# Performance work log

Hardware: AMD Instinct MI355X
Metric: run time of the kernel (lower is better)

Reference implementation:

```python
import jax, jax.numpy as jnp
import numpy as np

B, C, K, HH, WW, D = 2, 4, 32, 96, 96, 64


def setup_inputs() -> dict:
    key = jax.random.key(0)
    k1, k2, k3, k4, k5 = jax.random.split(key, 5)
    heatmaps = jax.random.uniform(k1, (B, C, K, HH, WW), dtype=jnp.float32)
    # Projection matrices: random linear part, translation column centered at
    # (H/2, W/2, 1) so that most cube points project inside the heatmap with z>0.
    P = 5.0 * jax.random.normal(k2, (B, C, 3, 4), dtype=jnp.float32)
    center = jnp.array([HH / 2.0, WW / 2.0, 1.0], dtype=jnp.float32)
    P = P.at[:, :, :, 3].set(center + 0.1 * jax.random.normal(k3, (B, C, 3)))
    coord_cubes = jax.random.uniform(k4, (B, D, D, D, 3), dtype=jnp.float32,
                                     minval=-1.0, maxval=1.0)
    vol_confidences = jax.random.uniform(k5, (B, C, K), dtype=jnp.float32) + 0.1
    return {
        "heatmaps": heatmaps,
        "projection_matrices": P,
        "coord_cubes": coord_cubes,
        "vol_confidences": vol_confidences,
    }


def _unproject(heatmaps, P, coord_cubes, conf):
    """Vectorized port of `unprojection` with agg_type='conf'.

    heatmaps: (B,C,K,H,W); P: (B,C,3,4); coord_cubes: (B,D,D,D,3); conf: (B,C,K)
    Returns volumes (B,K,D,D,D).
    """
    b, c, k, H, W = heatmaps.shape
    d = coord_cubes.shape[1]
    n = d * d * d
    coords = coord_cubes.reshape(b, n, 3)
    homo = jnp.concatenate([coords, jnp.ones((b, n, 1), coords.dtype)], axis=-1)
    # Projective transform per camera: (B,C,N,3)
    proj = jnp.einsum('bnj,bcij->bcni', homo, P)
    z = proj[..., 2]
    invalid = z <= 0.0
    z_safe = jnp.where(z == 0.0, 1.0, z)
    u = proj[..., 0] / z_safe
    v = proj[..., 1] / z_safe
    # Normalization exactly as in the source (x divided by H, y by W)
    gx = 2.0 * (u / H - 0.5)
    gy = 2.0 * (v / W - 0.5)
    # grid_sample align_corners=True: x indexes width, y indexes height
    ix = (gx + 1.0) * 0.5 * (W - 1)
    iy = (gy + 1.0) * 0.5 * (H - 1)
    x0 = jnp.floor(ix)
    y0 = jnp.floor(iy)
    x1 = x0 + 1.0
    y1 = y0 + 1.0
    wx1 = ix - x0
    wx0 = 1.0 - wx1
    wy1 = iy - y0
    wy0 = 1.0 - wy1
    hm = heatmaps.reshape(b, c, k, H * W)

    def corner(xc, yc, w):
        inb = (xc >= 0) & (xc <= W - 1) & (yc >= 0) & (yc <= H - 1)
        xi = jnp.clip(xc, 0, W - 1).astype(jnp.int32)
        yi = jnp.clip(yc, 0, H - 1).astype(jnp.int32)
        idx = (yi * W + xi)[:, :, None, :]                  # (B,C,1,N)
        idx = jnp.broadcast_to(idx, (b, c, k, idx.shape[-1]))
        g = jnp.take_along_axis(hm, idx, axis=3)            # (B,C,K,N)
        return g * (w * inb)[:, :, None, :]

    val = (corner(x0, y0, wx0 * wy0) + corner(x1, y0, wx1 * wy0)
           + corner(x0, y1, wx0 * wy1) + corner(x1, y1, wx1 * wy1))
    val = jnp.where(invalid[:, :, None, :], 0.0, val)       # zero invalid voxels
    # 'conf' aggregation; confidences normalized over cameras as in forward()
    conf_n = conf / conf.sum(axis=1, keepdims=True)
    vol = (val * conf_n[..., None]).sum(axis=1)             # (B,K,N)
    return vol.reshape(b, k, d, d, d)


def reference(heatmaps, projection_matrices, coord_cubes, vol_confidences):
    return _unproject(heatmaps, projection_matrices, coord_cubes, vol_confidences)
```

## Files before the change

### kernel.cpp

```cpp
#include <hip/hip_runtime.h>
#include <hip/hip_bf16.h>

#define BB 2
#define CC 4
#define KK 32
#define HHH 96
#define WWW 96
#define DDD 64
#define NN (DDD * DDD * DDD)
#define HWSZ (HHH * WWW)

__global__ __launch_bounds__(256) void hm_transpose(const float* __restrict__ in,
                                                    float* __restrict__ out) {
  __shared__ float tile[KK][64 + 1];
  const int bc  = blockIdx.y;
  const int hw0 = blockIdx.x * 64;
  const int t   = threadIdx.x;

  const float* src = in + (size_t)bc * KK * HWSZ;
  const int lhw = t & 63, lk0 = t >> 6;
#pragma unroll
  for (int i = 0; i < 8; ++i) {
    const int k = lk0 + i * 4;
    tile[k][lhw] = src[(size_t)k * HWSZ + hw0 + lhw];
  }
  __syncthreads();

  float* dst = out + ((size_t)bc * HWSZ + hw0) * KK;
  const int lk = t & 31, lh0 = t >> 5;
#pragma unroll
  for (int i = 0; i < 8; ++i) {
    const int h = lh0 + i * 8;
    dst[(size_t)h * KK + lk] = tile[lk][h];
  }
}

__global__ __launch_bounds__(256) void unproject3(
    const float* __restrict__ hmT,
    const float* __restrict__ Pm,
    const float* __restrict__ coords,
    const float* __restrict__ conf,
    float* __restrict__ out) {
  __shared__ float  sP[CC * 12];
  __shared__ float  sConf[CC][KK];
  __shared__ int4   sOff[CC][256];
  __shared__ float4 sW[CC][256];
  __shared__ float  vtile[32][KK + 1];

  const int t     = threadIdx.x;
  const int vbase = blockIdx.x * 256;
  const int b     = vbase >> 18;
  const int nbase = vbase & (NN - 1);

  if (t < CC * 12) sP[t] = Pm[b * CC * 12 + t];
  if (t < KK) {
    const float c0 = conf[(b * CC + 0) * KK + t];
    const float c1 = conf[(b * CC + 1) * KK + t];
    const float c2 = conf[(b * CC + 2) * KK + t];
    const float c3 = conf[(b * CC + 3) * KK + t];
    const float s  = c0 + c1 + c2 + c3;
    sConf[0][t] = c0 / s;
    sConf[1][t] = c1 / s;
    sConf[2][t] = c2 / s;
    sConf[3][t] = c3 / s;
  }
  __syncthreads();

  {
    const float x = coords[(size_t)(vbase + t) * 3 + 0];
    const float y = coords[(size_t)(vbase + t) * 3 + 1];
    const float z = coords[(size_t)(vbase + t) * 3 + 2];
    const float sxc = (float)(WWW - 1) / (float)HHH;
    const float syc = (float)(HHH - 1) / (float)WWW;
#pragma unroll
    for (int c = 0; c < CC; ++c) {
      const float* P = &sP[c * 12];
      const float pz = P[8] * x + P[9] * y + P[10] * z + P[11];
      const float valid = (pz > 0.0f) ? 1.0f : 0.0f;
      const float zs    = (pz > 0.0f) ? pz : 1.0f;
      const float px = P[0] * x + P[1] * y + P[2] * z + P[3];
      const float py = P[4] * x + P[5] * y + P[6] * z + P[7];
      const float u = px / zs, v2 = py / zs;
      const float ix = u * sxc, iy = v2 * syc;
      const float x0f = floorf(ix), y0f = floorf(iy);
      const float x1f = x0f + 1.0f, y1f = y0f + 1.0f;
      const float wx1 = ix - x0f, wx0 = 1.0f - wx1;
      const float wy1 = iy - y0f, wy0 = 1.0f - wy1;
      const float ibx0 = (x0f >= 0.f && x0f <= (float)(WWW - 1)) ? 1.f : 0.f;
      const float ibx1 = (x1f >= 0.f && x1f <= (float)(WWW - 1)) ? 1.f : 0.f;
      const float iby0 = (y0f >= 0.f && y0f <= (float)(HHH - 1)) ? 1.f : 0.f;
      const float iby1 = (y1f >= 0.f && y1f <= (float)(HHH - 1)) ? 1.f : 0.f;
      const int x0i = (int)fminf(fmaxf(x0f, 0.f), (float)(WWW - 1));
      const int x1i = (int)fminf(fmaxf(x1f, 0.f), (float)(WWW - 1));
      const int y0i = (int)fminf(fmaxf(y0f, 0.f), (float)(HHH - 1));
      const int y1i = (int)fminf(fmaxf(y1f, 0.f), (float)(HHH - 1));
      sOff[c][t] = make_int4(y0i * WWW + x0i, y0i * WWW + x1i,
                             y1i * WWW + x0i, y1i * WWW + x1i);
      sW[c][t] = make_float4(wx0 * wy0 * (ibx0 * iby0 * valid),
                             wx1 * wy0 * (ibx1 * iby0 * valid),
                             wx0 * wy1 * (ibx0 * iby1 * valid),
                             wx1 * wy1 * (ibx1 * iby1 * valid));
    }
  }
  __syncthreads();

  const int vloc = t >> 3;
  const int j    = t & 7;

  float4 cf[CC];
#pragma unroll
  for (int c = 0; c < CC; ++c) cf[c] = ((const float4*)sConf[c])[j];

  const float* base0 = hmT + (size_t)b * CC * HWSZ * KK + j * 4;
  float* ob = out + (size_t)b * KK * NN + nbase;

  for (int pass = 0; pass < 8; ++pass) {
    const int v = pass * 32 + vloc;
    float4 acc = make_float4(0.f, 0.f, 0.f, 0.f);
#pragma unroll
    for (int c = 0; c < CC; ++c) {
      const float4 w = sW[c][v];
      if (w.x + w.y + w.z + w.w > 0.0f) {
        const int4 off = sOff[c][v];
        const float* bc = base0 + (size_t)c * HWSZ * KK;
        const float4 g00 = *(const float4*)(bc + (size_t)off.x * KK);
        const float4 g01 = *(const float4*)(bc + (size_t)off.y * KK);
        const float4 g10 = *(const float4*)(bc + (size_t)off.z * KK);
        const float4 g11 = *(const float4*)(bc + (size_t)off.w * KK);
        acc.x += (g00.x * w.x + g01.x * w.y + g10.x * w.z + g11.x * w.w) * cf[c].x;
        acc.y += (g00.y * w.x + g01.y * w.y + g10.y * w.z + g11.y * w.w) * cf[c].y;
        acc.z += (g00.z * w.x + g01.z * w.y + g10.z * w.z + g11.z * w.w) * cf[c].z;
        acc.w += (g00.w * w.x + g01.w * w.y + g10.w * w.z + g11.w * w.w) * cf[c].w;
      }
    }
    vtile[vloc][j * 4 + 0] = acc.x;
    vtile[vloc][j * 4 + 1] = acc.y;
    vtile[vloc][j * 4 + 2] = acc.z;
    vtile[vloc][j * 4 + 3] = acc.w;
    __syncthreads();
#pragma unroll
    for (int q = 0; q < 4; ++q) {
      const int idx = t + q * 256;
      const int k   = idx >> 5;
      const int n0  = idx & 31;
      ob[(size_t)k * NN + pass * 32 + n0] = vtile[n0][k];
    }
    __syncthreads();
  }
}

__global__ __launch_bounds__(256) void unproject_native(
    const float* __restrict__ hm, const float* __restrict__ Pm,
    const float* __restrict__ coords, const float* __restrict__ conf,
    float* __restrict__ out) {
  __shared__ float sP[CC * 12];
  __shared__ float sConf[CC * KK];
  const int t   = threadIdx.x;
  const int gid = blockIdx.x * 256 + t;
  const int b   = gid >> 18;
  const int n   = gid & (NN - 1);
  if (t < CC * 12) sP[t] = Pm[b * CC * 12 + t];
  if (t < KK) {
    const float c0 = conf[(b * CC + 0) * KK + t];
    const float c1 = conf[(b * CC + 1) * KK + t];
    const float c2 = conf[(b * CC + 2) * KK + t];
    const float c3 = conf[(b * CC + 3) * KK + t];
    const float s  = c0 + c1 + c2 + c3;
    sConf[0 * KK + t] = c0 / s; sConf[1 * KK + t] = c1 / s;
    sConf[2 * KK + t] = c2 / s; sConf[3 * KK + t] = c3 / s;
  }
  __syncthreads();
  const float x = coords[(size_t)gid * 3 + 0];
  const float y = coords[(size_t)gid * 3 + 1];
  const float z = coords[(size_t)gid * 3 + 2];
  float accs[KK];
#pragma unroll
  for (int k = 0; k < KK; ++k) accs[k] = 0.f;
  const float sxc = (float)(WWW - 1) / (float)HHH;
  const float syc = (float)(HHH - 1) / (float)WWW;
#pragma unroll
  for (int c = 0; c < CC; ++c) {
    const float* P = &sP[c * 12];
    const float pz = P[8] * x + P[9] * y + P[10] * z + P[11];
    if (pz > 0.0f) {
      const float px = P[0] * x + P[1] * y + P[2] * z + P[3];
      const float py = P[4] * x + P[5] * y + P[6] * z + P[7];
      const float u = px / pz, v2 = py / pz;
      const float ix = u * sxc, iy = v2 * syc;
      const float x0f = floorf(ix), y0f = floorf(iy);
      const float x1f = x0f + 1.0f, y1f = y0f + 1.0f;
      const float wx1 = ix - x0f, wx0 = 1.0f - wx1;
      const float wy1 = iy - y0f, wy0 = 1.0f - wy1;
      const float ibx0 = (x0f >= 0.f && x0f <= (float)(WWW - 1)) ? 1.f : 0.f;
      const float ibx1 = (x1f >= 0.f && x1f <= (float)(WWW - 1)) ? 1.f : 0.f;
      const float iby0 = (y0f >= 0.f && y0f <= (float)(HHH - 1)) ? 1.f : 0.f;
      const float iby1 = (y1f >= 0.f && y1f <= (float)(HHH - 1)) ? 1.f : 0.f;
      const float w00 = wx0 * wy0 * ibx0 * iby0;
      const float w01 = wx1 * wy0 * ibx1 * iby0;
      const float w10 = wx0 * wy1 * ibx0 * iby1;
      const float w11 = wx1 * wy1 * ibx1 * iby1;
      const int x0i = (int)fminf(fmaxf(x0f, 0.f), (float)(WWW - 1));
      const int x1i = (int)fminf(fmaxf(x1f, 0.f), (float)(WWW - 1));
      const int y0i = (int)fminf(fmaxf(y0f, 0.f), (float)(HHH - 1));
      const int y1i = (int)fminf(fmaxf(y1f, 0.f), (float)(HHH - 1));
      const float* bse = hm + (size_t)(b * CC + c) * KK * HWSZ;
      const int i00 = y0i * WWW + x0i, i01 = y0i * WWW + x1i;
      const int i10 = y1i * WWW + x0i, i11 = y1i * WWW + x1i;
#pragma unroll
      for (int k = 0; k < KK; ++k) {
        const float* hk = bse + (size_t)k * HWSZ;
        accs[k] += (hk[i00] * w00 + hk[i01] * w01 +
                    hk[i10] * w10 + hk[i11] * w11) * sConf[c * KK + k];
      }
    }
  }
  float* ob = out + (size_t)b * KK * NN + n;
#pragma unroll
  for (int k = 0; k < KK; ++k) ob[(size_t)k * NN] = accs[k];
}

extern "C" void kernel_launch(void* const* d_in, const int* in_sizes, int n_in,
                              void* d_out, int out_size, void* d_ws, size_t ws_size,
                              hipStream_t stream) {
  const float* heatmaps = (const float*)d_in[0];
  const float* Pm       = (const float*)d_in[1];
  const float* coords   = (const float*)d_in[2];
  const float* conf     = (const float*)d_in[3];
  float* out            = (float*)d_out;

  const size_t hmT_bytes = (size_t)BB * CC * HWSZ * KK * sizeof(float);

  if (ws_size >= hmT_bytes) {
    float* hmT = (float*)d_ws;
    dim3 tg(HWSZ / 64, BB * CC);
    hm_transpose<<<tg, 256, 0, stream>>>(heatmaps, hmT);
    const int grid = (BB * NN) / 256;
    unproject3<<<grid, 256, 0, stream>>>(hmT, Pm, coords, conf, out);
  } else {
    const int grid = (BB * NN) / 256;
    unproject_native<<<grid, 256, 0, stream>>>(heatmaps, Pm, coords, conf, out);
  }
}
```

Measured before the change: 122.0 us.

## Store transposed heatmaps in fp16 and pack bilinear corner offsets

The transposed heatmap workspace is now stored as half precision, which halves the bytes each bilinear gather reads (8-byte loads instead of 16) and shrinks the cache footprint of the 2.4MB table. Corner offsets are packed into one 32-bit word (base index plus dx/dy bits), replacing an int4 per voxel/camera in shared memory. The cost is fp16 rounding of the heatmap values, which may exceed tight tolerances, plus extra conversion instructions.

```diff
diff --git a/kernel.cpp b/kernel.cpp
--- a/kernel.cpp
+++ b/kernel.cpp
@@ -1,5 +1,6 @@
 #include <hip/hip_runtime.h>
 #include <hip/hip_bf16.h>
+#include <hip/hip_fp16.h>
 
 #define BB 2
 #define CC 4
@@ -10,8 +11,8 @@
 #define NN (DDD * DDD * DDD)
 #define HWSZ (HHH * WWW)
 
-__global__ __launch_bounds__(256) void hm_transpose(const float* __restrict__ in,
-                                                    float* __restrict__ out) {
+__global__ __launch_bounds__(256) void hm_transpose_h(const float* __restrict__ in,
+                                                      __half* __restrict__ out) {
   __shared__ float tile[KK][64 + 1];
   const int bc  = blockIdx.y;
   const int hw0 = blockIdx.x * 64;
@@ -26,26 +27,28 @@
   }
   __syncthreads();
 
-  float* dst = out + ((size_t)bc * HWSZ + hw0) * KK;
-  const int lk = t & 31, lh0 = t >> 5;
-#pragma unroll
-  for (int i = 0; i < 8; ++i) {
-    const int h = lh0 + i * 8;
-    dst[(size_t)h * KK + lk] = tile[lk][h];
-  }
-}
-
-__global__ __launch_bounds__(256) void unproject3(
-    const float* __restrict__ hmT,
+  __half* dst = out + ((size_t)bc * HWSZ + hw0) * KK;
+  const int kp = (t & 15) * 2;
+  const int h0 = t >> 4;
+#pragma unroll
+  for (int i = 0; i < 4; ++i) {
+    const int h = h0 + i * 16;
+    const __half2 hv = __floats2half2_rn(tile[kp][h], tile[kp + 1][h]);
+    *(__half2*)(dst + (size_t)h * KK + kp) = hv;
+  }
+}
+
+__global__ __launch_bounds__(256) void unproject4(
+    const __half* __restrict__ hmT,
     const float* __restrict__ Pm,
     const float* __restrict__ coords,
     const float* __restrict__ conf,
     float* __restrict__ out) {
-  __shared__ float  sP[CC * 12];
-  __shared__ float  sConf[CC][KK];
-  __shared__ int4   sOff[CC][256];
-  __shared__ float4 sW[CC][256];
-  __shared__ float  vtile[32][KK + 1];
+  __shared__ float        sP[CC * 12];
+  __shared__ float        sConf[CC][KK];
+  __shared__ unsigned int sOffP[CC][256];
+  __shared__ float4       sW[CC][256];
+  __shared__ float        vtile[32][KK + 1];
 
   const int t     = threadIdx.x;
   const int vbase = blockIdx.x * 256;
@@ -94,8 +97,9 @@
       const int x1i = (int)fminf(fmaxf(x1f, 0.f), (float)(WWW - 1));
       const int y0i = (int)fminf(fmaxf(y0f, 0.f), (float)(HHH - 1));
       const int y1i = (int)fminf(fmaxf(y1f, 0.f), (float)(HHH - 1));
-      sOff[c][t] = make_int4(y0i * WWW + x0i, y0i * WWW + x1i,
-                             y1i * WWW + x0i, y1i * WWW + x1i);
+      sOffP[c][t] = (unsigned int)(y0i * WWW + x0i) |
+                    ((unsigned int)(x1i - x0i) << 14) |
+                    ((unsigned int)(y1i - y0i) << 15);
       sW[c][t] = make_float4(wx0 * wy0 * (ibx0 * iby0 * valid),
                              wx1 * wy0 * (ibx1 * iby0 * valid),
                              wx0 * wy1 * (ibx0 * iby1 * valid),
@@ -111,7 +115,7 @@
 #pragma unroll
   for (int c = 0; c < CC; ++c) cf[c] = ((const float4*)sConf[c])[j];
 
-  const float* base0 = hmT + (size_t)b * CC * HWSZ * KK + j * 4;
+  const __half* base0 = hmT + (size_t)b * CC * HWSZ * KK + j * 4;
   float* ob = out + (size_t)b * KK * NN + nbase;
 
   for (int pass = 0; pass < 8; ++pass) {
@@ -121,16 +125,27 @@
     for (int c = 0; c < CC; ++c) {
       const float4 w = sW[c][v];
       if (w.x + w.y + w.z + w.w > 0.0f) {
-        const int4 off = sOff[c][v];
-        const float* bc = base0 + (size_t)c * HWSZ * KK;
-        const float4 g00 = *(const float4*)(bc + (size_t)off.x * KK);
-        const float4 g01 = *(const float4*)(bc + (size_t)off.y * KK);
-        const float4 g10 = *(const float4*)(bc + (size_t)off.z * KK);
-        const float4 g11 = *(const float4*)(bc + (size_t)off.w * KK);
-        acc.x += (g00.x * w.x + g01.x * w.y + g10.x * w.z + g11.x * w.w) * cf[c].x;
-        acc.y += (g00.y * w.x + g01.y * w.y + g10.y * w.z + g11.y * w.w) * cf[c].y;
-        acc.z += (g00.z * w.x + g01.z * w.y + g10.z * w.z + g11.z * w.w) * cf[c].z;
-        acc.w += (g00.w * w.x + g01.w * w.y + g10.w * w.z + g11.w * w.w) * cf[c].w;
+        const unsigned int p = sOffP[c][v];
+        const int o00 = (int)(p & 0x3FFFu);
+        const int dx  = (int)((p >> 14) & 1u);
+        const int dyo = (int)((p >> 15) & 1u) * WWW;
+        const __half* hp = base0 + (size_t)c * (HWSZ * KK);
+        const uint2 q00 = *(const uint2*)(hp + (size_t)o00 * KK);
+        const uint2 q01 = *(const uint2*)(hp + (size_t)(o00 + dx) * KK);
+        const uint2 q10 = *(const uint2*)(hp + (size_t)(o00 + dyo) * KK);
+        const uint2 q11 = *(const uint2*)(hp + (size_t)(o00 + dyo + dx) * KK);
+        const float2 f00a = __half22float2(*(const __half2*)&q00.x);
+        const float2 f00b = __half22float2(*(const __half2*)&q00.y);
+        const float2 f01a = __half22float2(*(const __half2*)&q01.x);
+        const float2 f01b = __half22float2(*(const __half2*)&q01.y);
+        const float2 f10a = __half22float2(*(const __half2*)&q10.x);
+        const float2 f10b = __half22float2(*(const __half2*)&q10.y);
+        const float2 f11a = __half22float2(*(const __half2*)&q11.x);
+        const float2 f11b = __half22float2(*(const __half2*)&q11.y);
+        acc.x += (f00a.x * w.x + f01a.x * w.y + f10a.x * w.z + f11a.x * w.w) * cf[c].x;
+        acc.y += (f00a.y * w.x + f01a.y * w.y + f10a.y * w.z + f11a.y * w.w) * cf[c].y;
+        acc.z += (f00b.x * w.x + f01b.x * w.y + f10b.x * w.z + f11b.x * w.w) * cf[c].z;
+        acc.w += (f00b.y * w.x + f01b.y * w.y + f10b.y * w.z + f11b.y * w.w) * cf[c].w;
       }
     }
     vtile[vloc][j * 4 + 0] = acc.x;
@@ -228,14 +243,14 @@
   const float* conf     = (const float*)d_in[3];
   float* out            = (float*)d_out;
 
-  const size_t hmT_bytes = (size_t)BB * CC * HWSZ * KK * sizeof(float);
+  const size_t hmT_bytes = (size_t)BB * CC * HWSZ * KK * sizeof(__half);
 
   if (ws_size >= hmT_bytes) {
-    float* hmT = (float*)d_ws;
+    __half* hmT = (__half*)d_ws;
     dim3 tg(HWSZ / 64, BB * CC);
-    hm_transpose<<<tg, 256, 0, stream>>>(heatmaps, hmT);
+    hm_transpose_h<<<tg, 256, 0, stream>>>(heatmaps, hmT);
     const int grid = (BB * NN) / 256;
-    unproject3<<<grid, 256, 0, stream>>>(hmT, Pm, coords, conf, out);
+    unproject4<<<grid, 256, 0, stream>>>(hmT, Pm, coords, conf, out);
   } else {
     const int grid = (BB * NN) / 256;
     unproject_native<<<grid, 256, 0, stream>>>(heatmaps, Pm, coords, conf, out);
```

After: 123.8 us. About the same (+1.4%).
